# Kernel optimization log

Hardware: AMD Instinct MI355X
Metric: run time of the kernel (lower is better)

## Reference

```python
import jax, jax.numpy as jnp
import numpy as np

N, E, IN_DIM, HID, LAYERS = 300000, 600000, 64, 128, 2
BN_EPS = 1e-5

def setup_inputs() -> dict:
    key = jax.random.key(0)
    ks = jax.random.split(key, 8)
    scale_in = 1.0 / np.sqrt(IN_DIM)
    scale_h = 1.0 / np.sqrt(HID)
    return {
        "node_init": jax.random.normal(ks[0], (N, IN_DIM), dtype=jnp.float32),
        "edge_index": jax.random.randint(ks[1], (2, E), 0, N, dtype=jnp.int64),
        "edge_len": jax.random.uniform(ks[2], (E,), dtype=jnp.float32),
        "W_in": jax.random.normal(ks[3], (IN_DIM, HID), dtype=jnp.float32) * scale_in,
        "b_in": jnp.zeros((HID,), dtype=jnp.float32),
        "att_k": jax.random.normal(ks[4], (HID,), dtype=jnp.float32),
        "Wl": jax.random.normal(ks[5], (LAYERS, HID, HID), dtype=jnp.float32) * scale_h,
        "bl": jnp.zeros((LAYERS, HID), dtype=jnp.float32),
        "gamma": jnp.ones((LAYERS, HID), dtype=jnp.float32),
        "beta": jnp.zeros((LAYERS, HID), dtype=jnp.float32),
    }

def reference(node_init, edge_index, edge_len, W_in, b_in, att_k, Wl, bl, gamma, beta):
    src, dst = edge_index[0], edge_index[1]
    inv_len = 1.0 / (1.0 + edge_len)                     # [E]
    inv_sqrt_h = 1.0 / jnp.sqrt(jnp.asarray(HID, node_init.dtype))
    h = node_init @ W_in + b_in                          # [N,H]
    n = h.shape[0]
    for l in range(LAYERS):
        h_src = h[src]                                   # [E,H] gather
        key = (h_src @ att_k) * inv_sqrt_h               # [E]
        w = jnp.exp(key) * inv_len                       # [E]
        agg = jax.ops.segment_sum(w[:, None] * h_src, dst, num_segments=n)  # [N,H]
        h = h + jax.nn.relu(agg) @ Wl[l] + bl[l]
        mean = jnp.mean(h, axis=0)
        var = jnp.mean((h - mean) ** 2, axis=0)          # biased var (BatchNorm training)
        h = (h - mean) * jax.lax.rsqrt(var + BN_EPS) * gamma[l] + beta[l]
    return h
```

## Files before the change

### kernel.cpp

```cpp
#include <hip/hip_runtime.h>
#include <hip/hip_bf16.h>

#define N_NODES 300000
#define N_EDGES 600000
#define IN_DIMC 64
#define HIDC    128
#define NLAYERS 2
#define BN_EPS  1e-5f
#define INV_SQRT_H 0.08838834764831845f
#define NB_SCAN ((N_NODES + 255) / 256)
#define NTILES  (N_NODES / 16)

typedef __bf16 bf16x8 __attribute__((ext_vector_type(8)));
typedef float floatx4 __attribute__((ext_vector_type(4)));

__device__ int   g_row_ptr[N_NODES + 1];
__device__ int   g_cursor[N_NODES];
__device__ __align__(8) int2 g_edge[N_EDGES];
__device__ int   g_bsum[NB_SCAN];
__device__ float g_ekey[N_NODES];
__device__ __align__(16) __hip_bfloat16 g_Win_hi[128 * 64];
__device__ __align__(16) __hip_bfloat16 g_Win_lo[128 * 64];
__device__ __align__(16) __hip_bfloat16 g_Wl_hi[NLAYERS * 128 * 128];
__device__ __align__(16) __hip_bfloat16 g_Wl_lo[NLAYERS * 128 * 128];
__device__ float g_stats[NLAYERS * 2 * HIDC];
__device__ __align__(16) float g_bn_sc[NLAYERS * HIDC];
__device__ __align__(16) float g_bn_sh[NLAYERS * HIDC];

__device__ inline void split2(float x, __hip_bfloat16& hi, __hip_bfloat16& lo) {
    hi = __float2bfloat16(x);
    lo = __float2bfloat16(x - __bfloat162float(hi));
}

__global__ void zero_kernel() {
    int i = blockIdx.x * 256 + threadIdx.x;
    if (i < N_NODES) g_cursor[i] = 0;
    if (i < NLAYERS * 2 * HIDC) g_stats[i] = 0.f;
}

__global__ void prep_w_kernel(const float* __restrict__ W_in,
                              const float* __restrict__ Wl)
{
    int id = blockIdx.x * 256 + threadIdx.x;
    if (id < 128 * 64) {
        int n = id >> 6, k = id & 63;
        split2(W_in[k * 128 + n], g_Win_hi[id], g_Win_lo[id]);
    }
    if (id < NLAYERS * 128 * 128) {
        int l = id >> 14, r = id & 16383;
        int n = r >> 7, k = r & 127;
        split2(Wl[l * 16384 + k * 128 + n], g_Wl_hi[id], g_Wl_lo[id]);
    }
}

__global__ void hist_kernel(const int* __restrict__ dst)
{
    int e = blockIdx.x * 256 + threadIdx.x;
    if (e < N_EDGES) atomicAdd(&g_cursor[dst[e]], 1);
}

__global__ void scan1_kernel()
{
    __shared__ int tmp[256];
    int t = threadIdx.x;
    int i = blockIdx.x * 256 + t;
    tmp[t] = (i < N_NODES) ? g_cursor[i] : 0;
    __syncthreads();
    for (int d = 128; d > 0; d >>= 1) {
        if (t < d) tmp[t] += tmp[t + d];
        __syncthreads();
    }
    if (t == 0) g_bsum[blockIdx.x] = tmp[0];
}

__global__ void scan2_kernel()
{
    __shared__ int tmp[256];
    __shared__ int carry;
    int t = threadIdx.x;
    if (t == 0) { carry = 0; g_row_ptr[N_NODES] = N_EDGES; }
    __syncthreads();
    for (int base = 0; base < NB_SCAN; base += 256) {
        int i = base + t;
        int v = (i < NB_SCAN) ? g_bsum[i] : 0;
        tmp[t] = v;
        __syncthreads();
        for (int d = 1; d < 256; d <<= 1) {
            int x = (t >= d) ? tmp[t - d] : 0;
            __syncthreads();
            tmp[t] += x;
            __syncthreads();
        }
        int c = carry;
        if (i < NB_SCAN) g_bsum[i] = c + tmp[t] - v;
        __syncthreads();
        if (t == 0) carry = c + tmp[255];
        __syncthreads();
    }
}

__global__ void scan3_kernel()
{
    __shared__ int tmp[256];
    int t = threadIdx.x;
    int i = blockIdx.x * 256 + t;
    int v = (i < N_NODES) ? g_cursor[i] : 0;
    tmp[t] = v;
    __syncthreads();
    for (int d = 1; d < 256; d <<= 1) {
        int x = (t >= d) ? tmp[t - d] : 0;
        __syncthreads();
        tmp[t] += x;
        __syncthreads();
    }
    int r = g_bsum[blockIdx.x] + tmp[t] - v;
    if (i < N_NODES) { g_row_ptr[i] = r; g_cursor[i] = r; }
}

__global__ void scatter_kernel(const int* __restrict__ src, const int* __restrict__ dst,
                               const float* __restrict__ elen)
{
    int e = blockIdx.x * 256 + threadIdx.x;
    if (e >= N_EDGES) return;
    int d = dst[e];
    int pos = atomicAdd(&g_cursor[d], 1);
    int2 ed;
    ed.x = src[e];
    ed.y = __float_as_int(1.0f / (1.0f + elen[e]));
    g_edge[pos] = ed;
}

__global__ __launch_bounds__(256) void edge_csr_kernel(
    const float* __restrict__ h, float* __restrict__ agg, int prev)
{
    int lane = threadIdx.x & 63;
    int n = blockIdx.x * 4 + (threadIdx.x >> 6);
    if (n >= N_NODES) return;
    int beg = g_row_ptr[n], end = g_row_ptr[n + 1];
    float a0 = 0.f, a1 = 0.f, sw = 0.f;
    const float2* h2 = (const float2*)h;
    int j = beg;
    for (; j + 1 < end; j += 2) {
        int2 e0 = g_edge[j];
        int2 e1 = g_edge[j + 1];
        float w0 = g_ekey[e0.x] * __int_as_float(e0.y);
        float w1 = g_ekey[e1.x] * __int_as_float(e1.y);
        float2 x0 = h2[(size_t)e0.x * 64 + lane];
        float2 x1 = h2[(size_t)e1.x * 64 + lane];
        a0 += w0 * x0.x + w1 * x1.x;
        a1 += w0 * x0.y + w1 * x1.y;
        sw += w0 + w1;
    }
    if (j < end) {
        int2 e0 = g_edge[j];
        float w0 = g_ekey[e0.x] * __int_as_float(e0.y);
        float2 x0 = h2[(size_t)e0.x * 64 + lane];
        a0 += w0 * x0.x;
        a1 += w0 * x0.y;
        sw += w0;
    }
    float2 sc = make_float2(1.f, 1.f), sh = make_float2(0.f, 0.f);
    if (prev >= 0) {
        sc = ((const float2*)(g_bn_sc + prev * HIDC))[lane];
        sh = ((const float2*)(g_bn_sh + prev * HIDC))[lane];
    }
    float2 o;
    o.x = fmaxf(sc.x * a0 + sh.x * sw, 0.f);
    o.y = fmaxf(sc.y * a1 + sh.y * sw, 0.f);
    ((float2*)(agg + (size_t)n * HIDC))[lane] = o;
}

__global__ __launch_bounds__(256) void proj_mfma_kernel(
    const float* __restrict__ X, const float* __restrict__ b,
    const float* __restrict__ att_k, float* __restrict__ h)
{
    __shared__ __align__(16) __hip_bfloat16 Ah[64 * 72];
    __shared__ __align__(16) __hip_bfloat16 Al[64 * 72];
    __shared__ __align__(16) __hip_bfloat16 Bh[128 * 72];
    __shared__ __align__(16) __hip_bfloat16 Bl[128 * 72];
    int t = threadIdx.x;
    int nbase = blockIdx.x * 64;

    for (int i = t; i < 1024; i += 256) {
        int row = i >> 3, c8 = i & 7;
        *(float4*)((char*)Bh + row * 144 + c8 * 16) =
            *(const float4*)((const char*)g_Win_hi + row * 128 + c8 * 16);
        *(float4*)((char*)Bl + row * 144 + c8 * 16) =
            *(const float4*)((const char*)g_Win_lo + row * 128 + c8 * 16);
    }
    for (int i = t; i < 1024; i += 256) {
        int row = i >> 4, c4 = i & 15;
        int n = nbase + row;
        float4 v = make_float4(0.f, 0.f, 0.f, 0.f);
        if (n < N_NODES) v = *(const float4*)(X + (size_t)n * IN_DIMC + c4 * 4);
        union { __hip_bfloat16 e[4]; uint2 u; } ph, pl;
        split2(v.x, ph.e[0], pl.e[0]); split2(v.y, ph.e[1], pl.e[1]);
        split2(v.z, ph.e[2], pl.e[2]); split2(v.w, ph.e[3], pl.e[3]);
        *(uint2*)((char*)Ah + row * 144 + c4 * 8) = ph.u;
        *(uint2*)((char*)Al + row * 144 + c4 * 8) = pl.u;
    }
    __syncthreads();

    int lane = t & 63, w = t >> 6;
    int m16 = lane & 15, quad = lane >> 4;
    floatx4 acc[8];
#pragma unroll
    for (int i = 0; i < 8; ++i) acc[i] = floatx4{0.f, 0.f, 0.f, 0.f};

#pragma unroll
    for (int kk = 0; kk < 64; kk += 32) {
        bf16x8 ah = *(const bf16x8*)((const char*)Ah + (w * 16 + m16) * 144 + (kk + quad * 8) * 2);
        bf16x8 al = *(const bf16x8*)((const char*)Al + (w * 16 + m16) * 144 + (kk + quad * 8) * 2);
#pragma unroll
        for (int nt = 0; nt < 8; ++nt) {
            bf16x8 bh = *(const bf16x8*)((const char*)Bh + (nt * 16 + m16) * 144 + (kk + quad * 8) * 2);
            bf16x8 bl = *(const bf16x8*)((const char*)Bl + (nt * 16 + m16) * 144 + (kk + quad * 8) * 2);
            acc[nt] = __builtin_amdgcn_mfma_f32_16x16x32_bf16(ah, bh, acc[nt], 0, 0, 0);
            acc[nt] = __builtin_amdgcn_mfma_f32_16x16x32_bf16(al, bh, acc[nt], 0, 0, 0);
            acc[nt] = __builtin_amdgcn_mfma_f32_16x16x32_bf16(ah, bl, acc[nt], 0, 0, 0);
        }
    }
    float dotr[4] = {0.f, 0.f, 0.f, 0.f};
#pragma unroll
    for (int nt = 0; nt < 8; ++nt) {
        int ch = nt * 16 + m16;
        float bias = b[ch];
        float ak = att_k[ch];
#pragma unroll
        for (int r = 0; r < 4; ++r) {
            int n = nbase + w * 16 + quad * 4 + r;
            float o = acc[nt][r] + bias;
            if (n < N_NODES) h[(size_t)n * HIDC + ch] = o;
            dotr[r] += ak * o;
        }
    }
#pragma unroll
    for (int r = 0; r < 4; ++r) {
        float p = dotr[r];
        p += __shfl_xor(p, 1); p += __shfl_xor(p, 2);
        p += __shfl_xor(p, 4); p += __shfl_xor(p, 8);
        int n = nbase + w * 16 + quad * 4 + r;
        if (m16 == 0 && n < N_NODES) g_ekey[n] = __expf(p * INV_SQRT_H);
    }
}

__global__ __launch_bounds__(256) void key_kernel(const float* __restrict__ h,
                                                  const float* __restrict__ att_k,
                                                  int prev)
{
    int t = threadIdx.x;
    int lane = t & 63;
    int half = lane >> 5, sub = lane & 31;
    int n = (blockIdx.x * 4 + (t >> 6)) * 2 + half;
    if (n >= N_NODES) return;
    float4 x = ((const float4*)h)[(size_t)n * 32 + sub];
    float4 sc = ((const float4*)(g_bn_sc + prev * HIDC))[sub];
    float4 sh = ((const float4*)(g_bn_sh + prev * HIDC))[sub];
    float4 ak = ((const float4*)att_k)[sub];
    float p = (sc.x * x.x + sh.x) * ak.x + (sc.y * x.y + sh.y) * ak.y +
              (sc.z * x.z + sh.z) * ak.z + (sc.w * x.w + sh.w) * ak.w;
    p += __shfl_xor(p, 1);  p += __shfl_xor(p, 2);
    p += __shfl_xor(p, 4);  p += __shfl_xor(p, 8);
    p += __shfl_xor(p, 16);
    if (sub == 0) g_ekey[n] = __expf(p * INV_SQRT_H);
}

__global__ __launch_bounds__(256) void layer_gemm_kernel(
    float* __restrict__ h, const float* __restrict__ agg,
    const float* __restrict__ b, int layer, int prev)
{
    __shared__ __align__(16) __hip_bfloat16 Bh[128 * 136];
    __shared__ __align__(16) __hip_bfloat16 Bl[128 * 136];
    __shared__ float red[256];
    int t = threadIdx.x;
    const __hip_bfloat16* Wh = g_Wl_hi + layer * 16384;
    const __hip_bfloat16* Wlo = g_Wl_lo + layer * 16384;
    red[t] = 0.f;

    for (int i = t; i < 2048; i += 256) {
        int row = i >> 4, c8 = i & 15;
        *(float4*)((char*)Bh + row * 272 + c8 * 16) =
            *(const float4*)((const char*)Wh + row * 256 + c8 * 16);
        *(float4*)((char*)Bl + row * 272 + c8 * 16) =
            *(const float4*)((const char*)Wlo + row * 256 + c8 * 16);
    }
    __syncthreads();

    const int lane = t & 63, w = t >> 6;
    const int m16 = lane & 15, quad = lane >> 4;
    const int wid = blockIdx.x * 4 + w;
    const int nwaves = gridDim.x * 4;

    float bias[8], scp[8], shp[8];
#pragma unroll
    for (int nt = 0; nt < 8; ++nt) {
        int ch = nt * 16 + m16;
        bias[nt] = b[ch];
        scp[nt] = (prev >= 0) ? g_bn_sc[prev * HIDC + ch] : 1.f;
        shp[nt] = (prev >= 0) ? g_bn_sh[prev * HIDC + ch] : 0.f;
    }
    float sreg[8], qreg[8];
#pragma unroll
    for (int nt = 0; nt < 8; ++nt) { sreg[nt] = 0.f; qreg[nt] = 0.f; }

    for (int tile = wid; tile < NTILES; tile += nwaves) {
        const float* arow = agg + (size_t)(tile * 16 + m16) * HIDC + quad * 8;
        floatx4 acc[8];
#pragma unroll
        for (int i = 0; i < 8; ++i) acc[i] = floatx4{0.f, 0.f, 0.f, 0.f};

#pragma unroll
        for (int kk = 0; kk < 4; ++kk) {
            float4 a0 = *(const float4*)(arow + kk * 32);
            float4 a1 = *(const float4*)(arow + kk * 32 + 4);
            union { __hip_bfloat16 e[8]; bf16x8 v; } ah, al;
            split2(a0.x, ah.e[0], al.e[0]); split2(a0.y, ah.e[1], al.e[1]);
            split2(a0.z, ah.e[2], al.e[2]); split2(a0.w, ah.e[3], al.e[3]);
            split2(a1.x, ah.e[4], al.e[4]); split2(a1.y, ah.e[5], al.e[5]);
            split2(a1.z, ah.e[6], al.e[6]); split2(a1.w, ah.e[7], al.e[7]);
#pragma unroll
            for (int nt = 0; nt < 8; ++nt) {
                bf16x8 bh = *(const bf16x8*)((const char*)Bh + (nt * 16 + m16) * 272 + (kk * 32 + quad * 8) * 2);
                bf16x8 bl = *(const bf16x8*)((const char*)Bl + (nt * 16 + m16) * 272 + (kk * 32 + quad * 8) * 2);
                acc[nt] = __builtin_amdgcn_mfma_f32_16x16x32_bf16(ah.v, bh, acc[nt], 0, 0, 0);
                acc[nt] = __builtin_amdgcn_mfma_f32_16x16x32_bf16(al.v, bh, acc[nt], 0, 0, 0);
                acc[nt] = __builtin_amdgcn_mfma_f32_16x16x32_bf16(ah.v, bl, acc[nt], 0, 0, 0);
            }
        }
        int node0 = tile * 16 + quad * 4;
#pragma unroll
        for (int nt = 0; nt < 8; ++nt) {
            int ch = nt * 16 + m16;
#pragma unroll
            for (int r = 0; r < 4; ++r) {
                float* hp = h + (size_t)(node0 + r) * HIDC + ch;
                float o = scp[nt] * (*hp) + shp[nt] + acc[nt][r] + bias[nt];
                *hp = o;
                sreg[nt] += o;
                qreg[nt] += o * o;
            }
        }
    }

#pragma unroll
    for (int nt = 0; nt < 8; ++nt) {
        float s = sreg[nt], q = qreg[nt];
        s += __shfl_xor(s, 16); s += __shfl_xor(s, 32);
        q += __shfl_xor(q, 16); q += __shfl_xor(q, 32);
        if (quad == 0) {
            atomicAdd(&red[nt * 16 + m16], s);
            atomicAdd(&red[HIDC + nt * 16 + m16], q);
        }
    }
    __syncthreads();
    atomicAdd(&g_stats[layer * 2 * HIDC + t], red[t]);
}

__global__ void bn_prep_kernel(const float* __restrict__ gamma,
                               const float* __restrict__ beta, int layer)
{
    int c = threadIdx.x;
    if (c >= HIDC) return;
    const float invN = 1.0f / (float)N_NODES;
    float mean = g_stats[layer * 2 * HIDC + c] * invN;
    float var = g_stats[layer * 2 * HIDC + HIDC + c] * invN - mean * mean;
    float s = gamma[layer * HIDC + c] * rsqrtf(var + BN_EPS);
    g_bn_sc[layer * HIDC + c] = s;
    g_bn_sh[layer * HIDC + c] = beta[layer * HIDC + c] - mean * s;
}

__global__ __launch_bounds__(256) void bn_apply_kernel(float* __restrict__ h, int layer)
{
    size_t idx = (size_t)blockIdx.x * 256 + threadIdx.x;
    if (idx >= (size_t)N_NODES * (HIDC / 4)) return;
    int cg = (int)(idx & 31);
    float4 sc = ((const float4*)(g_bn_sc + layer * HIDC))[cg];
    float4 sh = ((const float4*)(g_bn_sh + layer * HIDC))[cg];
    float4 v = ((float4*)h)[idx];
    v.x = sc.x * v.x + sh.x;
    v.y = sc.y * v.y + sh.y;
    v.z = sc.z * v.z + sh.z;
    v.w = sc.w * v.w + sh.w;
    ((float4*)h)[idx] = v;
}

extern "C" void kernel_launch(void* const* d_in, const int* in_sizes, int n_in,
                              void* d_out, int out_size, void* d_ws, size_t ws_size,
                              hipStream_t stream) {
    (void)in_sizes; (void)n_in; (void)out_size; (void)ws_size;
    const float* node_init = (const float*)d_in[0];
    const int*   eidx      = (const int*)d_in[1];
    const float* elen      = (const float*)d_in[2];
    const float* W_in      = (const float*)d_in[3];
    const float* b_in      = (const float*)d_in[4];
    const float* att_k     = (const float*)d_in[5];
    const float* Wl        = (const float*)d_in[6];
    const float* bl        = (const float*)d_in[7];
    const float* gamma     = (const float*)d_in[8];
    const float* beta      = (const float*)d_in[9];

    float* h   = (float*)d_out;
    float* agg = (float*)d_ws;

    const int* src = eidx;
    const int* dst = eidx + N_EDGES;

    zero_kernel<<<NB_SCAN, 256, 0, stream>>>();
    hist_kernel<<<(N_EDGES + 255) / 256, 256, 0, stream>>>(dst);
    scan1_kernel<<<NB_SCAN, 256, 0, stream>>>();
    scan2_kernel<<<1, 256, 0, stream>>>();
    scan3_kernel<<<NB_SCAN, 256, 0, stream>>>();
    scatter_kernel<<<(N_EDGES + 255) / 256, 256, 0, stream>>>(src, dst, elen);
    prep_w_kernel<<<(NLAYERS * 128 * 128 + 255) / 256, 256, 0, stream>>>(W_in, Wl);

    proj_mfma_kernel<<<(N_NODES + 63) / 64, 256, 0, stream>>>(node_init, b_in, att_k, h);

    for (int l = 0; l < NLAYERS; ++l) {
        if (l > 0)
            key_kernel<<<(N_NODES / 2 + 3) / 4, 256, 0, stream>>>(h, att_k, l - 1);
        edge_csr_kernel<<<(N_NODES + 3) / 4, 256, 0, stream>>>(h, agg, l - 1);
        layer_gemm_kernel<<<512, 256, 0, stream>>>(h, agg, bl + (size_t)l * HIDC, l, l - 1);
        bn_prep_kernel<<<1, 128, 0, stream>>>(gamma, beta, l);
    }
    bn_apply_kernel<<<(N_NODES * (HIDC / 4) + 255) / 256, 256, 0, stream>>>(h, NLAYERS - 1);
}
```

Baseline: 942.4 us.

## Fuse CSR edge aggregation into layer GEMM with double-buffered LDS tiles

Merges the per-node edge gather/aggregation and the MFMA layer GEMM into one persistent kernel. Each block gathers a 16-node tile into shared memory as split bf16 while computing the previous tile, and weights are held in registers per wave (one 16-channel slice each). This removes the agg intermediate's global write and read. It ping-pongs h between the output and workspace buffers to avoid in-place hazards. Risks: wave-level load imbalance from uneven degrees, since each wave loops to the larger degree of its two nodes, and lower gather parallelism per tile.

```diff
diff --git a/kernel.cpp b/kernel.cpp
--- a/kernel.cpp
+++ b/kernel.cpp
@@ -10,6 +10,7 @@
 #define INV_SQRT_H 0.08838834764831845f
 #define NB_SCAN ((N_NODES + 255) / 256)
 #define NTILES  (N_NODES / 16)
+#define FUSED_GRID 2048
 
 typedef __bf16 bf16x8 __attribute__((ext_vector_type(8)));
 typedef float floatx4 __attribute__((ext_vector_type(4)));
@@ -128,46 +129,6 @@
     ed.x = src[e];
     ed.y = __float_as_int(1.0f / (1.0f + elen[e]));
     g_edge[pos] = ed;
-}
-
-__global__ __launch_bounds__(256) void edge_csr_kernel(
-    const float* __restrict__ h, float* __restrict__ agg, int prev)
-{
-    int lane = threadIdx.x & 63;
-    int n = blockIdx.x * 4 + (threadIdx.x >> 6);
-    if (n >= N_NODES) return;
-    int beg = g_row_ptr[n], end = g_row_ptr[n + 1];
-    float a0 = 0.f, a1 = 0.f, sw = 0.f;
-    const float2* h2 = (const float2*)h;
-    int j = beg;
-    for (; j + 1 < end; j += 2) {
-        int2 e0 = g_edge[j];
-        int2 e1 = g_edge[j + 1];
-        float w0 = g_ekey[e0.x] * __int_as_float(e0.y);
-        float w1 = g_ekey[e1.x] * __int_as_float(e1.y);
-        float2 x0 = h2[(size_t)e0.x * 64 + lane];
-        float2 x1 = h2[(size_t)e1.x * 64 + lane];
-        a0 += w0 * x0.x + w1 * x1.x;
-        a1 += w0 * x0.y + w1 * x1.y;
-        sw += w0 + w1;
-    }
-    if (j < end) {
-        int2 e0 = g_edge[j];
-        float w0 = g_ekey[e0.x] * __int_as_float(e0.y);
-        float2 x0 = h2[(size_t)e0.x * 64 + lane];
-        a0 += w0 * x0.x;
-        a1 += w0 * x0.y;
-        sw += w0;
-    }
-    float2 sc = make_float2(1.f, 1.f), sh = make_float2(0.f, 0.f);
-    if (prev >= 0) {
-        sc = ((const float2*)(g_bn_sc + prev * HIDC))[lane];
-        sh = ((const float2*)(g_bn_sh + prev * HIDC))[lane];
-    }
-    float2 o;
-    o.x = fmaxf(sc.x * a0 + sh.x * sw, 0.f);
-    o.y = fmaxf(sc.y * a1 + sh.y * sw, 0.f);
-    ((float2*)(agg + (size_t)n * HIDC))[lane] = o;
 }
 
 __global__ __launch_bounds__(256) void proj_mfma_kernel(
@@ -265,95 +226,123 @@
     if (sub == 0) g_ekey[n] = __expf(p * INV_SQRT_H);
 }
 
-__global__ __launch_bounds__(256) void layer_gemm_kernel(
-    float* __restrict__ h, const float* __restrict__ agg,
+__global__ __launch_bounds__(512, 4) void fused_layer_kernel(
+    const float* __restrict__ h_old, float* __restrict__ h_new,
     const float* __restrict__ b, int layer, int prev)
 {
-    __shared__ __align__(16) __hip_bfloat16 Bh[128 * 136];
-    __shared__ __align__(16) __hip_bfloat16 Bl[128 * 136];
-    __shared__ float red[256];
-    int t = threadIdx.x;
-    const __hip_bfloat16* Wh = g_Wl_hi + layer * 16384;
-    const __hip_bfloat16* Wlo = g_Wl_lo + layer * 16384;
-    red[t] = 0.f;
-
-    for (int i = t; i < 2048; i += 256) {
-        int row = i >> 4, c8 = i & 15;
-        *(float4*)((char*)Bh + row * 272 + c8 * 16) =
-            *(const float4*)((const char*)Wh + row * 256 + c8 * 16);
-        *(float4*)((char*)Bl + row * 272 + c8 * 16) =
-            *(const float4*)((const char*)Wlo + row * 256 + c8 * 16);
-    }
-    __syncthreads();
-
+    __shared__ __align__(16) __hip_bfloat16 Ah[2][16][136];
+    __shared__ __align__(16) __hip_bfloat16 Al[2][16][136];
+
+    const int t = threadIdx.x;
     const int lane = t & 63, w = t >> 6;
     const int m16 = lane & 15, quad = lane >> 4;
-    const int wid = blockIdx.x * 4 + w;
-    const int nwaves = gridDim.x * 4;
-
-    float bias[8], scp[8], shp[8];
-#pragma unroll
-    for (int nt = 0; nt < 8; ++nt) {
-        int ch = nt * 16 + m16;
-        bias[nt] = b[ch];
-        scp[nt] = (prev >= 0) ? g_bn_sc[prev * HIDC + ch] : 1.f;
-        shp[nt] = (prev >= 0) ? g_bn_sh[prev * HIDC + ch] : 0.f;
-    }
-    float sreg[8], qreg[8];
-#pragma unroll
-    for (int nt = 0; nt < 8; ++nt) { sreg[nt] = 0.f; qreg[nt] = 0.f; }
-
-    for (int tile = wid; tile < NTILES; tile += nwaves) {
-        const float* arow = agg + (size_t)(tile * 16 + m16) * HIDC + quad * 8;
-        floatx4 acc[8];
-#pragma unroll
-        for (int i = 0; i < 8; ++i) acc[i] = floatx4{0.f, 0.f, 0.f, 0.f};
-
+    const int ch = w * 16 + m16;
+
+    bf16x8 bh[4], blo[4];
+    {
+        const __hip_bfloat16* Wh  = g_Wl_hi + layer * 16384 + ch * 128 + quad * 8;
+        const __hip_bfloat16* Wl2 = g_Wl_lo + layer * 16384 + ch * 128 + quad * 8;
 #pragma unroll
         for (int kk = 0; kk < 4; ++kk) {
-            float4 a0 = *(const float4*)(arow + kk * 32);
-            float4 a1 = *(const float4*)(arow + kk * 32 + 4);
-            union { __hip_bfloat16 e[8]; bf16x8 v; } ah, al;
-            split2(a0.x, ah.e[0], al.e[0]); split2(a0.y, ah.e[1], al.e[1]);
-            split2(a0.z, ah.e[2], al.e[2]); split2(a0.w, ah.e[3], al.e[3]);
-            split2(a1.x, ah.e[4], al.e[4]); split2(a1.y, ah.e[5], al.e[5]);
-            split2(a1.z, ah.e[6], al.e[6]); split2(a1.w, ah.e[7], al.e[7]);
-#pragma unroll
-            for (int nt = 0; nt < 8; ++nt) {
-                bf16x8 bh = *(const bf16x8*)((const char*)Bh + (nt * 16 + m16) * 272 + (kk * 32 + quad * 8) * 2);
-                bf16x8 bl = *(const bf16x8*)((const char*)Bl + (nt * 16 + m16) * 272 + (kk * 32 + quad * 8) * 2);
-                acc[nt] = __builtin_amdgcn_mfma_f32_16x16x32_bf16(ah.v, bh, acc[nt], 0, 0, 0);
-                acc[nt] = __builtin_amdgcn_mfma_f32_16x16x32_bf16(al.v, bh, acc[nt], 0, 0, 0);
-                acc[nt] = __builtin_amdgcn_mfma_f32_16x16x32_bf16(ah.v, bl, acc[nt], 0, 0, 0);
+            bh[kk]  = *(const bf16x8*)(Wh  + kk * 32);
+            blo[kk] = *(const bf16x8*)(Wl2 + kk * 32);
+        }
+    }
+
+    float bias = b[ch];
+    float scp = 1.f, shp = 0.f;
+    float2 scg = make_float2(1.f, 1.f), shg = make_float2(0.f, 0.f);
+    if (prev >= 0) {
+        scp = g_bn_sc[prev * HIDC + ch];
+        shp = g_bn_sh[prev * HIDC + ch];
+        scg = ((const float2*)(g_bn_sc + prev * HIDC))[lane];
+        shg = ((const float2*)(g_bn_sh + prev * HIDC))[lane];
+    }
+
+    const float2* h2 = (const float2*)h_old;
+    float sreg = 0.f, qreg = 0.f;
+
+    auto gather = [&](int tl, int buf) {
+        int n0 = tl * 16 + w * 2;
+        int rp0 = g_row_ptr[n0];
+        int rp1 = g_row_ptr[n0 + 1];
+        int rp2 = g_row_ptr[n0 + 2];
+        float a0x = 0.f, a0y = 0.f, s0 = 0.f;
+        float a1x = 0.f, a1y = 0.f, s1 = 0.f;
+        int j0 = rp0, j1 = rp1;
+        int d0 = rp1 - rp0, d1 = rp2 - rp1;
+        int rmax = d0 > d1 ? d0 : d1;
+        for (int r = 0; r < rmax; ++r) {
+            if (j0 < rp1) {
+                int2 E = g_edge[j0++];
+                float wt = g_ekey[E.x] * __int_as_float(E.y);
+                float2 x = h2[(size_t)E.x * 64 + lane];
+                a0x += wt * x.x; a0y += wt * x.y; s0 += wt;
             }
-        }
-        int node0 = tile * 16 + quad * 4;
-#pragma unroll
-        for (int nt = 0; nt < 8; ++nt) {
-            int ch = nt * 16 + m16;
-#pragma unroll
-            for (int r = 0; r < 4; ++r) {
-                float* hp = h + (size_t)(node0 + r) * HIDC + ch;
-                float o = scp[nt] * (*hp) + shp[nt] + acc[nt][r] + bias[nt];
-                *hp = o;
-                sreg[nt] += o;
-                qreg[nt] += o * o;
+            if (j1 < rp2) {
+                int2 E = g_edge[j1++];
+                float wt = g_ekey[E.x] * __int_as_float(E.y);
+                float2 x = h2[(size_t)E.x * 64 + lane];
+                a1x += wt * x.x; a1y += wt * x.y; s1 += wt;
             }
         }
-    }
-
-#pragma unroll
-    for (int nt = 0; nt < 8; ++nt) {
-        float s = sreg[nt], q = qreg[nt];
-        s += __shfl_xor(s, 16); s += __shfl_xor(s, 32);
-        q += __shfl_xor(q, 16); q += __shfl_xor(q, 32);
-        if (quad == 0) {
-            atomicAdd(&red[nt * 16 + m16], s);
-            atomicAdd(&red[HIDC + nt * 16 + m16], q);
-        }
-    }
+        float o0x = fmaxf(scg.x * a0x + shg.x * s0, 0.f);
+        float o0y = fmaxf(scg.y * a0y + shg.y * s0, 0.f);
+        float o1x = fmaxf(scg.x * a1x + shg.x * s1, 0.f);
+        float o1y = fmaxf(scg.y * a1y + shg.y * s1, 0.f);
+        union { __hip_bfloat16 e[2]; unsigned u; } p0h, p0l, p1h, p1l;
+        split2(o0x, p0h.e[0], p0l.e[0]); split2(o0y, p0h.e[1], p0l.e[1]);
+        split2(o1x, p1h.e[0], p1l.e[0]); split2(o1y, p1h.e[1], p1l.e[1]);
+        *(unsigned*)&Ah[buf][w * 2][2 * lane]     = p0h.u;
+        *(unsigned*)&Al[buf][w * 2][2 * lane]     = p0l.u;
+        *(unsigned*)&Ah[buf][w * 2 + 1][2 * lane] = p1h.u;
+        *(unsigned*)&Al[buf][w * 2 + 1][2 * lane] = p1l.u;
+    };
+
+    auto compute = [&](int tl, int buf) {
+        floatx4 acc = floatx4{0.f, 0.f, 0.f, 0.f};
+#pragma unroll
+        for (int kk = 0; kk < 4; ++kk) {
+            bf16x8 ah = *(const bf16x8*)&Ah[buf][m16][kk * 32 + quad * 8];
+            bf16x8 al = *(const bf16x8*)&Al[buf][m16][kk * 32 + quad * 8];
+            acc = __builtin_amdgcn_mfma_f32_16x16x32_bf16(ah, bh[kk],  acc, 0, 0, 0);
+            acc = __builtin_amdgcn_mfma_f32_16x16x32_bf16(al, bh[kk],  acc, 0, 0, 0);
+            acc = __builtin_amdgcn_mfma_f32_16x16x32_bf16(ah, blo[kk], acc, 0, 0, 0);
+        }
+        int node0 = tl * 16 + quad * 4;
+#pragma unroll
+        for (int r = 0; r < 4; ++r) {
+            size_t off = (size_t)(node0 + r) * HIDC + ch;
+            float o = scp * h_old[off] + shp + acc[r] + bias;
+            h_new[off] = o;
+            sreg += o; qreg += o * o;
+        }
+    };
+
+    int tile = blockIdx.x;
+    int cur = 0;
+    gather(tile, 0);
     __syncthreads();
-    atomicAdd(&g_stats[layer * 2 * HIDC + t], red[t]);
+    for (;;) {
+        int next = tile + (int)gridDim.x;
+        if (next < NTILES) {
+            gather(next, cur ^ 1);
+            compute(tile, cur);
+            __syncthreads();
+            tile = next;
+            cur ^= 1;
+        } else {
+            compute(tile, cur);
+            break;
+        }
+    }
+
+    sreg += __shfl_xor(sreg, 16); sreg += __shfl_xor(sreg, 32);
+    qreg += __shfl_xor(qreg, 16); qreg += __shfl_xor(qreg, 32);
+    if (quad == 0) {
+        atomicAdd(&g_stats[layer * 2 * HIDC + ch], sreg);
+        atomicAdd(&g_stats[layer * 2 * HIDC + HIDC + ch], qreg);
+    }
 }
 
 __global__ void bn_prep_kernel(const float* __restrict__ gamma,
@@ -399,8 +388,8 @@
     const float* gamma     = (const float*)d_in[8];
     const float* beta      = (const float*)d_in[9];
 
-    float* h   = (float*)d_out;
-    float* agg = (float*)d_ws;
+    float* hA = (float*)d_out;
+    float* hB = (float*)d_ws;
 
     const int* src = eidx;
     const int* dst = eidx + N_EDGES;
@@ -413,14 +402,14 @@
     scatter_kernel<<<(N_EDGES + 255) / 256, 256, 0, stream>>>(src, dst, elen);
     prep_w_kernel<<<(NLAYERS * 128 * 128 + 255) / 256, 256, 0, stream>>>(W_in, Wl);
 
-    proj_mfma_kernel<<<(N_NODES + 63) / 64, 256, 0, stream>>>(node_init, b_in, att_k, h);
-
-    for (int l = 0; l < NLAYERS; ++l) {
-        if (l > 0)
-            key_kernel<<<(N_NODES / 2 + 3) / 4, 256, 0, stream>>>(h, att_k, l - 1);
-        edge_csr_kernel<<<(N_NODES + 3) / 4, 256, 0, stream>>>(h, agg, l - 1);
-        layer_gemm_kernel<<<512, 256, 0, stream>>>(h, agg, bl + (size_t)l * HIDC, l, l - 1);
-        bn_prep_kernel<<<1, 128, 0, stream>>>(gamma, beta, l);
-    }
-    bn_apply_kernel<<<(N_NODES * (HIDC / 4) + 255) / 256, 256, 0, stream>>>(h, NLAYERS - 1);
-}
+    proj_mfma_kernel<<<(N_NODES + 63) / 64, 256, 0, stream>>>(node_init, b_in, att_k, hA);
+
+    fused_layer_kernel<<<FUSED_GRID, 512, 0, stream>>>(hA, hB, bl, 0, -1);
+    bn_prep_kernel<<<1, 128, 0, stream>>>(gamma, beta, 0);
+
+    key_kernel<<<(N_NODES / 2 + 3) / 4, 256, 0, stream>>>(hB, att_k, 0);
+    fused_layer_kernel<<<FUSED_GRID, 512, 0, stream>>>(hB, hA, bl + HIDC, 1, 0);
+    bn_prep_kernel<<<1, 128, 0, stream>>>(gamma, beta, 1);
+
+    bn_apply_kernel<<<(N_NODES * (HIDC / 4) + 255) / 256, 256, 0, stream>>>(hA, NLAYERS - 1);
+}
```

Result: slower. 1.030 ms (+9.3%).
